# Kernel optimization log

Measured on AMD Instinct MI355X. Metric: run time of the kernel, lower is better.

Reference implementation:

```python
import jax, jax.numpy as jnp
import numpy as np

B, N, D = 4, 2048, 512
H, DH = 8, 64
MLP = 2048
EPS = 1e-5


def setup_inputs() -> dict:
    key = jax.random.key(0)
    ks = jax.random.split(key, 8)
    s = lambda fan_in: 1.0 / np.sqrt(fan_in)
    return {
        "x": jax.random.normal(ks[0], (B, N, D), jnp.float32),
        "ln1_g": jnp.ones((D,), jnp.float32),
        "ln1_b": jnp.zeros((D,), jnp.float32),
        "Wqkv": jax.random.normal(ks[1], (D, 3 * H * DH), jnp.float32) * s(D),
        "temperature": jnp.asarray(np.log(DH ** -0.5), jnp.float32),
        "Wo": jax.random.normal(ks[2], (H * DH, D), jnp.float32) * s(H * DH),
        "bo": jnp.zeros((D,), jnp.float32),
        "ln2_g": jnp.ones((D,), jnp.float32),
        "ln2_b": jnp.zeros((D,), jnp.float32),
        "W1": jax.random.normal(ks[3], (D, MLP), jnp.float32) * s(D),
        "b1": jnp.zeros((MLP,), jnp.float32),
        "W2": jax.random.normal(ks[4], (MLP, D), jnp.float32) * s(MLP),
        "b2": jnp.zeros((D,), jnp.float32),
    }


def _layernorm(x, g, b):
    mu = jnp.mean(x, axis=-1, keepdims=True)
    var = jnp.var(x, axis=-1, keepdims=True)
    return (x - mu) * jax.lax.rsqrt(var + EPS) * g + b


def _lsa(x, Wqkv, temperature, Wo, bo):
    b, n, _ = x.shape
    qkv = x @ Wqkv  # [b, n, 3*H*DH]
    q, k, v = jnp.split(qkv, 3, axis=-1)
    rs = lambda t: t.reshape(b, n, H, DH).transpose(0, 2, 1, 3)  # b h n d
    q, k, v = rs(q), rs(k), rs(v)
    dots = jnp.einsum("bhnd,bhmd->bhnm", q, k) * jnp.exp(temperature)
    mask_value = -jnp.finfo(dots.dtype).max
    eye = jnp.eye(n, dtype=bool)
    dots = jnp.where(eye, mask_value, dots)  # mask diagonal (LSA)
    attn = jax.nn.softmax(dots, axis=-1)
    out = jnp.einsum("bhnm,bhmd->bhnd", attn, v)
    out = out.transpose(0, 2, 1, 3).reshape(b, n, H * DH)
    return out @ Wo + bo


def _ffn(x, W1, b1, W2, b2):
    h = jax.nn.gelu(x @ W1 + b1, approximate=False)
    return h @ W2 + b2


def reference(x, ln1_g, ln1_b, Wqkv, temperature, Wo, bo,
              ln2_g, ln2_b, W1, b1, W2, b2):
    y = _lsa(_layernorm(x, ln1_g, ln1_b), Wqkv, temperature, Wo, bo) + x
    z = _ffn(_layernorm(y, ln2_g, ln2_b), W1, b1, W2, b2) + y
    return (z, x)
```

## Files before the change

kernel.cpp:

```cpp
#include <hip/hip_runtime.h>
#include <math.h>

typedef __attribute__((ext_vector_type(4))) float f32x4;
typedef __attribute__((ext_vector_type(8))) short short8;

#define DEV __device__ __forceinline__

DEV short f2bf(float f){
  union { float f; unsigned u; } v; v.f = f;
  unsigned r = v.u + 0x7fffu + ((v.u >> 16) & 1u);
  return (short)(r >> 16);
}
DEV float bf2f(short s){
  union { unsigned u; float f; } v; v.u = ((unsigned)(unsigned short)s) << 16; return v.f;
}
DEV float exp2_hw(float x){ float r; asm("v_exp_f32 %0, %1" : "=v"(r) : "v"(x)); return r; }
DEV float rcp_hw(float x){ float r; asm("v_rcp_f32 %0, %1" : "=v"(r) : "v"(x)); return r; }
DEV unsigned cvtpk(float a, float b){
  unsigned r; asm("v_cvt_pk_bf16_f32 %0, %1, %2" : "=v"(r) : "v"(a), "v"(b)); return r;
}
DEV void gload_lds16(const short* src, short* lds){
  __builtin_amdgcn_global_load_lds(
      (const __attribute__((address_space(1))) void*)src,
      (__attribute__((address_space(3))) void*)lds, 16, 0, 0);
}

__global__ __launch_bounds__(256) void transpose_bf16_kernel(
    const float* __restrict__ W, short* __restrict__ Wt, int K, int N)
{
  __shared__ float tile[32][33];
  int nb = blockIdx.x * 32, kb = blockIdx.y * 32;
  int tx = threadIdx.x & 31, ty = threadIdx.x >> 5;
  #pragma unroll
  for (int i = ty; i < 32; i += 8)
    tile[i][tx] = W[(size_t)(kb + i) * N + nb + tx];
  __syncthreads();
  #pragma unroll
  for (int i = ty; i < 32; i += 8)
    Wt[(size_t)(nb + i) * K + kb + tx] = f2bf(tile[tx][i]);
}

template<int COPYX>
__global__ __launch_bounds__(256) void ln_kernel(
    const float* __restrict__ x, const float* __restrict__ g,
    const float* __restrict__ b, short* __restrict__ out,
    float* __restrict__ xcopy)
{
  int row  = blockIdx.x * 4 + (threadIdx.x >> 6);
  int lane = threadIdx.x & 63;
  const float* xr = x + (size_t)row * 512 + lane * 8;
  f32x4 v0 = *(const f32x4*)(xr);
  f32x4 v1 = *(const f32x4*)(xr + 4);
  float s  = (v0[0]+v0[1]+v0[2]+v0[3]) + (v1[0]+v1[1]+v1[2]+v1[3]);
  float sq = (v0[0]*v0[0]+v0[1]*v0[1]+v0[2]*v0[2]+v0[3]*v0[3])
           + (v1[0]*v1[0]+v1[1]*v1[1]+v1[2]*v1[2]+v1[3]*v1[3]);
  #pragma unroll
  for (int off = 1; off < 64; off <<= 1) {
    s  += __shfl_xor(s, off);
    sq += __shfl_xor(sq, off);
  }
  float mu  = s * (1.0f / 512.0f);
  float var = sq * (1.0f / 512.0f) - mu * mu;
  float rstd = rsqrtf(var + 1e-5f);
  f32x4 g0 = *(const f32x4*)(g + lane * 8);
  f32x4 g1 = *(const f32x4*)(g + lane * 8 + 4);
  f32x4 b0 = *(const f32x4*)(b + lane * 8);
  f32x4 b1 = *(const f32x4*)(b + lane * 8 + 4);
  float o[8];
  #pragma unroll
  for (int j = 0; j < 4; ++j) o[j]     = (v0[j] - mu) * rstd * g0[j] + b0[j];
  #pragma unroll
  for (int j = 0; j < 4; ++j) o[4 + j] = (v1[j] - mu) * rstd * g1[j] + b1[j];
  uint4 pk;
  pk.x = cvtpk(o[0], o[1]); pk.y = cvtpk(o[2], o[3]);
  pk.z = cvtpk(o[4], o[5]); pk.w = cvtpk(o[6], o[7]);
  *(uint4*)(out + (size_t)row * 512 + lane * 8) = pk;
  if (COPYX) {
    float* xc = xcopy + (size_t)row * 512 + lane * 8;
    *(f32x4*)(xc)     = v0;
    *(f32x4*)(xc + 4) = v1;
  }
}

template<int EPI, int BM, typename OutT>
__global__ __launch_bounds__(256) void gemm_bt_kernel(
    const short* __restrict__ A, const short* __restrict__ Bt,
    OutT* __restrict__ C, const float* __restrict__ bias,
    const float* __restrict__ resid, short* __restrict__ vt,
    int M, int N, int K)
{
  constexpr int MFR = BM / 32;
  constexpr int NFR = 4;
  constexpr int AI  = BM / 64;
  constexpr int BUF = BM * 32 + 128 * 32;
  __shared__ __align__(16) short smem[3 * BUF];

  int tid = threadIdx.x;
  int lane = tid & 63, wid = tid >> 6;
  int l16 = lane & 15, lq = lane >> 4;

  int gx = gridDim.x;
  int nwg = gx * gridDim.y;
  int orig = blockIdx.y * gx + blockIdx.x;
  int swz = (orig & 7) * (nwg >> 3) + (orig >> 3);
  int bn = swz % gx, bm = swz / gx;

  int wm = wid >> 1, wn = wid & 1;

  const short* gaP[AI];
  const short* gbP[2];
  #pragma unroll
  for (int i = 0; i < AI; ++i) {
    int gg = i * 4 + wid;
    gaP[i] = A + (size_t)(bm * BM + gg * 16 + l16) * K + lq * 8;
  }
  #pragma unroll
  for (int i = 0; i < 2; ++i) {
    int gg = i * 4 + wid;
    gbP[i] = Bt + (size_t)(bn * 128 + gg * 16 + l16) * K + lq * 8;
  }

  auto STAGE = [&](int bufi, int k0) {
    short* base = smem + bufi * BUF;
    #pragma unroll
    for (int i = 0; i < AI; ++i)
      gload_lds16(gaP[i] + k0, base + (i * 4 + wid) * 512);
    #pragma unroll
    for (int i = 0; i < 2; ++i)
      gload_lds16(gbP[i] + k0, base + BM * 32 + (i * 4 + wid) * 512);
  };

  f32x4 acc[MFR][NFR] = {};

  STAGE(0, 0);
  STAGE(1, 32);

  int nt = K >> 5;
  for (int t = 0; t < nt; ++t) {
    if (t + 1 < nt) {
      if constexpr (AI == 2) asm volatile("s_waitcnt vmcnt(4)" ::: "memory");
      else                   asm volatile("s_waitcnt vmcnt(3)" ::: "memory");
    } else {
      asm volatile("s_waitcnt vmcnt(0)" ::: "memory");
    }
    __builtin_amdgcn_s_barrier();
    __builtin_amdgcn_sched_barrier(0);
    if (t + 2 < nt) STAGE((t + 2) % 3, (t + 2) << 5);

    const short* base = smem + (t % 3) * BUF;
    short8 af[MFR], bfr[NFR];
    #pragma unroll
    for (int m = 0; m < MFR; ++m)
      af[m] = *(const short8*)(base + (wm * MFR + m) * 512 + lane * 8);
    #pragma unroll
    for (int n = 0; n < NFR; ++n)
      bfr[n] = *(const short8*)(base + BM * 32 + (wn * NFR + n) * 512 + lane * 8);
    __builtin_amdgcn_s_setprio(1);
    #pragma unroll
    for (int m = 0; m < MFR; ++m)
      #pragma unroll
      for (int n = 0; n < NFR; ++n)
        acc[m][n] = __builtin_amdgcn_mfma_f32_16x16x32_bf16(af[m], bfr[n], acc[m][n], 0, 0, 0);
    __builtin_amdgcn_s_setprio(0);
  }

  if (EPI == 3 && bn >= 8) {
    __syncthreads();
    short* T = smem;
    #pragma unroll
    for (int m = 0; m < MFR; ++m)
      #pragma unroll
      for (int n = 0; n < NFR; ++n) {
        int c = wn * 64 + n * 16 + l16;
        #pragma unroll
        for (int r = 0; r < 4; ++r) {
          int rowl = wm * 64 + m * 16 + lq * 4 + r;
          T[c * 128 + (rowl ^ ((c & 7) << 4))] = f2bf(acc[m][n][r]);
        }
      }
    __syncthreads();
    int b2 = bm >> 4;
    int nnb = (bm & 15) * 128;
    int tn = tid & 15;
    #pragma unroll
    for (int c8 = 0; c8 < 8; ++c8) {
      int c = c8 * 16 + (tid >> 4);
      short8 v = *(const short8*)(T + c * 128 + ((tn * 8) ^ ((c & 7) << 4)));
      if (tn & 1) {
        short8 w;
        #pragma unroll
        for (int j = 0; j < 8; ++j) w[j] = v[j ^ 4];
        v = w;
      }
      int c2 = bn * 128 + c - 1024;
      int bh = b2 * 8 + (c2 >> 6);
      int d  = c2 & 63;
      *(short8*)(vt + ((size_t)(bh * 64 + d)) * 2048 + nnb + tn * 8) = v;
    }
    return;
  }

  float bv[NFR];
  #pragma unroll
  for (int n = 0; n < NFR; ++n)
    bv[n] = (EPI == 0 || EPI == 3) ? 0.0f : bias[bn * 128 + (wn * NFR + n) * 16 + l16];

  #pragma unroll
  for (int m = 0; m < MFR; ++m) {
    #pragma unroll
    for (int r = 0; r < 4; ++r) {
      int row = bm * BM + (wm * MFR + m) * 16 + lq * 4 + r;
      #pragma unroll
      for (int n = 0; n < NFR; ++n) {
        int col = bn * 128 + (wn * NFR + n) * 16 + l16;
        float v = acc[m][n][r];
        if (EPI == 1 || EPI == 2) v += bv[n];
        if (EPI == 2) v = 0.5f * v * (1.0f + erff(v * 0.70710678f));
        if (EPI == 1) v += resid[(size_t)row * N + col];
        if constexpr (sizeof(OutT) == 2)
          ((short*)C)[(size_t)row * N + col] = f2bf(v);
        else
          ((float*)C)[(size_t)row * N + col] = v;
      }
    }
  }
}

__global__ __launch_bounds__(256, 2) void attn_kernel(
    const short* __restrict__ qkv, const short* __restrict__ vt,
    const float* __restrict__ temp_ptr, short* __restrict__ out)
{
  __shared__ __align__(16) short smem[24576];

  int tid = threadIdx.x;
  int lane = tid & 63, wid = tid >> 6;
  int l16 = lane & 15, lq = lane >> 4;
  int hi = lq >> 1, lq0 = lq & 1;

  int orig = blockIdx.y * 16 + blockIdx.x;
  int swz = (orig & 7) * 64 + (orig >> 3);
  int qb = swz & 15, bh = swz >> 4;
  int b = bh >> 3, h = bh & 7;

  const short* qbase = qkv + (size_t)b * 2048 * 1536 + h * 64;
  const short* kbase = qbase + 512;
  const short* vbase = vt + (size_t)bh * 64 * 2048;

  float scale = __expf(temp_ptr[0]) * 1.44269504f;
  int q0 = qb * 128 + wid * 32;

  short8 qfrag[2][2];
  #pragma unroll
  for (int qf = 0; qf < 2; ++qf) {
    int qrow = q0 + qf * 16 + l16;
    #pragma unroll
    for (int c = 0; c < 2; ++c) {
      short8 raw = *(const short8*)(qbase + (size_t)qrow * 1536 + c * 32 + lq * 8);
      short8 sc;
      #pragma unroll
      for (int j = 0; j < 8; ++j) sc[j] = f2bf(bf2f(raw[j]) * scale);
      qfrag[qf][c] = sc;
    }
  }

  f32x4 accO[2][4] = {};
  float l[2] = {0.f, 0.f};

  auto STAGE = [&](int bufi, int k0) {
    #pragma unroll
    for (int i = 0; i < 2; ++i) {
      int w16 = i * 256 + tid;
      int sub = w16 >> 7;
      int cc  = (w16 >> 6) & 1;
      int lq2 = (w16 >> 4) & 3;
      int l2  = w16 & 15;
      const short* srcK = kbase + (size_t)(k0 + sub * 16 + l2) * 1536 + cc * 32 + lq2 * 8;
      gload_lds16(srcK, smem + bufi * 4096 + (i * 4 + wid) * 512);
      const short* srcV = vbase + (size_t)(sub * 16 + l2) * 2048 + k0 + cc * 32 + lq2 * 8;
      gload_lds16(srcV, smem + 12288 + bufi * 4096 + (i * 4 + wid) * 512);
    }
  };

  STAGE(0, 0);
  STAGE(1, 64);

  for (int t = 0; t < 32; ++t) {
    if (t + 1 < 32) asm volatile("s_waitcnt vmcnt(4)" ::: "memory");
    else            asm volatile("s_waitcnt vmcnt(0)" ::: "memory");
    __builtin_amdgcn_s_barrier();
    __builtin_amdgcn_sched_barrier(0);
    if (t + 2 < 32) STAGE((t + 2) % 3, (t + 2) * 64);

    int k0 = t * 64;
    const short* kls = smem + (t % 3) * 4096;
    const short* vls = smem + 12288 + (t % 3) * 4096;

    f32x4 accS[2][4] = {};
    __builtin_amdgcn_s_setprio(1);
    #pragma unroll
    for (int s = 0; s < 4; ++s) {
      short8 kf0 = *(const short8*)(kls + (s * 2 + 0) * 512 + lane * 8);
      short8 kf1 = *(const short8*)(kls + (s * 2 + 1) * 512 + lane * 8);
      #pragma unroll
      for (int qf = 0; qf < 2; ++qf) {
        accS[qf][s] = __builtin_amdgcn_mfma_f32_16x16x32_bf16(kf0, qfrag[qf][0], accS[qf][s], 0, 0, 0);
        accS[qf][s] = __builtin_amdgcn_mfma_f32_16x16x32_bf16(kf1, qfrag[qf][1], accS[qf][s], 0, 0, 0);
      }
    }
    __builtin_amdgcn_s_setprio(0);

    if ((q0 & ~63) == k0) {
      #pragma unroll
      for (int qf = 0; qf < 2; ++qf) {
        int qg = q0 + qf * 16 + l16;
        #pragma unroll
        for (int s = 0; s < 4; ++s)
          #pragma unroll
          for (int r = 0; r < 4; ++r)
            if (k0 + s * 16 + lq * 4 + r == qg) accS[qf][s][r] = -30000.f;
      }
    }

    short8 pa[2][2];
    #pragma unroll
    for (int qf = 0; qf < 2; ++qf) {
      float sum = 0.f;
      unsigned W[4][2];
      #pragma unroll
      for (int s = 0; s < 4; ++s) {
        float p0 = exp2_hw(accS[qf][s][0]);
        float p1 = exp2_hw(accS[qf][s][1]);
        float p2 = exp2_hw(accS[qf][s][2]);
        float p3 = exp2_hw(accS[qf][s][3]);
        sum += (p0 + p1) + (p2 + p3);
        W[s][0] = cvtpk(p0, p1);
        W[s][1] = cvtpk(p2, p3);
      }
      sum += __shfl_xor(sum, 16);
      sum += __shfl_xor(sum, 32);
      l[qf] += sum;

      unsigned K0[2], S0[2], K2[2], S2[2], R0[2], R2[2];
      #pragma unroll
      for (int w = 0; w < 2; ++w) {
        K0[w] = hi ? W[1][w] : W[0][w];
        S0[w] = hi ? W[0][w] : W[1][w];
        K2[w] = hi ? W[3][w] : W[2][w];
        S2[w] = hi ? W[2][w] : W[3][w];
      }
      #pragma unroll
      for (int w = 0; w < 2; ++w) {
        R0[w] = (unsigned)__shfl_xor((int)S0[w], 32);
        R2[w] = (unsigned)__shfl_xor((int)S2[w], 32);
      }
      bool sw = (hi != lq0);
      unsigned FA[2], FB[2], sA[2], sB[2], GA[2], GB[2];
      #pragma unroll
      for (int w = 0; w < 2; ++w) {
        sA[w] = sw ? K0[w] : R0[w];  FA[w] = sw ? R0[w] : K0[w];
        sB[w] = sw ? K2[w] : R2[w];  FB[w] = sw ? R2[w] : K2[w];
      }
      #pragma unroll
      for (int w = 0; w < 2; ++w) {
        GA[w] = (unsigned)__shfl_xor((int)sA[w], 16);
        GB[w] = (unsigned)__shfl_xor((int)sB[w], 16);
      }
      union { unsigned u[4]; short8 s8; } p0u, p1u;
      p0u.u[0] = FA[0]; p0u.u[1] = FA[1]; p0u.u[2] = GA[0]; p0u.u[3] = GA[1];
      p1u.u[0] = FB[0]; p1u.u[1] = FB[1]; p1u.u[2] = GB[0]; p1u.u[3] = GB[1];
      pa[qf][0] = p0u.s8;
      pa[qf][1] = p1u.s8;
    }

    short8 vfr[4][2];
    #pragma unroll
    for (int d = 0; d < 4; ++d) {
      vfr[d][0] = *(const short8*)(vls + (d * 2 + 0) * 512 + lane * 8);
      vfr[d][1] = *(const short8*)(vls + (d * 2 + 1) * 512 + lane * 8);
    }
    __builtin_amdgcn_s_setprio(1);
    #pragma unroll
    for (int qf = 0; qf < 2; ++qf)
      #pragma unroll
      for (int d = 0; d < 4; ++d) {
        accO[qf][d] = __builtin_amdgcn_mfma_f32_16x16x32_bf16(vfr[d][0], pa[qf][0], accO[qf][d], 0, 0, 0);
        accO[qf][d] = __builtin_amdgcn_mfma_f32_16x16x32_bf16(vfr[d][1], pa[qf][1], accO[qf][d], 0, 0, 0);
      }
    __builtin_amdgcn_s_setprio(0);
  }

  #pragma unroll
  for (int qf = 0; qf < 2; ++qf) {
    float inv = rcp_hw(l[qf]);
    int qg = q0 + qf * 16 + l16;
    size_t rowoff = (size_t)(b * 2048 + qg) * 512 + h * 64;
    #pragma unroll
    for (int d = 0; d < 4; ++d) {
      unsigned w0 = cvtpk(accO[qf][d][0] * inv, accO[qf][d][1] * inv);
      unsigned w1 = cvtpk(accO[qf][d][2] * inv, accO[qf][d][3] * inv);
      uint2 pk; pk.x = w0; pk.y = w1;
      *(uint2*)(out + rowoff + d * 16 + lq * 4) = pk;
    }
  }
}

extern "C" void kernel_launch(void* const* d_in, const int* in_sizes, int n_in,
                              void* d_out, int out_size, void* d_ws, size_t ws_size,
                              hipStream_t stream)
{
  const float* x    = (const float*)d_in[0];
  const float* ln1g = (const float*)d_in[1];
  const float* ln1b = (const float*)d_in[2];
  const float* Wqkv = (const float*)d_in[3];
  const float* temp = (const float*)d_in[4];
  const float* Wo   = (const float*)d_in[5];
  const float* bo   = (const float*)d_in[6];
  const float* ln2g = (const float*)d_in[7];
  const float* ln2b = (const float*)d_in[8];
  const float* W1   = (const float*)d_in[9];
  const float* b1   = (const float*)d_in[10];
  const float* W2   = (const float*)d_in[11];
  const float* b2   = (const float*)d_in[12];
  float* out = (float*)d_out;

  char* ws = (char*)d_ws;
  short* wqkv_t = (short*)(ws);
  short* wo_t   = (short*)(ws + 1572864);
  short* w1_t   = (short*)(ws + 2097152);
  short* w2_t   = (short*)(ws + 4194304);
  short* h      = (short*)(ws + 6291456);
  short* qkv    = (short*)(ws + 14680064);
  short* attn   = (short*)(ws + 39845888);
  float* y      = (float*)(ws + 48234496);
  short* vt     = (short*)(ws + 48234496);
  short* t      = (short*)(ws + 14680064);

  const int M = 8192;

  transpose_bf16_kernel<<<dim3(1536 / 32, 512 / 32),  256, 0, stream>>>(Wqkv, wqkv_t, 512, 1536);
  transpose_bf16_kernel<<<dim3(512 / 32, 512 / 32),   256, 0, stream>>>(Wo,   wo_t,   512, 512);
  transpose_bf16_kernel<<<dim3(2048 / 32, 512 / 32),  256, 0, stream>>>(W1,   w1_t,   512, 2048);
  transpose_bf16_kernel<<<dim3(512 / 32, 2048 / 32),  256, 0, stream>>>(W2,   w2_t,   2048, 512);

  ln_kernel<1><<<M / 4, 256, 0, stream>>>(x, ln1g, ln1b, h, out + (size_t)M * 512);

  gemm_bt_kernel<3, 128, short><<<dim3(1536 / 128, M / 128), 256, 0, stream>>>(
      h, wqkv_t, qkv, nullptr, nullptr, vt, M, 1536, 512);

  attn_kernel<<<dim3(16, 32), 256, 0, stream>>>(qkv, vt, temp, attn);

  gemm_bt_kernel<1, 64, float><<<dim3(512 / 128, M / 64), 256, 0, stream>>>(
      attn, wo_t, y, bo, x, nullptr, M, 512, 512);

  ln_kernel<0><<<M / 4, 256, 0, stream>>>(y, ln2g, ln2b, h, nullptr);

  gemm_bt_kernel<2, 128, short><<<dim3(2048 / 128, M / 128), 256, 0, stream>>>(
      h, w1_t, t, b1, nullptr, nullptr, M, 2048, 512);

  gemm_bt_kernel<1, 64, float><<<dim3(512 / 128, M / 64), 256, 0, stream>>>(
      t, w2_t, out, b2, y, nullptr, M, 512, 2048);
}
```

Before: 223.9 us.

## Load K/V fragments directly from global into registers in attention kernel

Removes the LDS triple-buffered staging of K and V tiles with global_load_lds and barriers, and has each wave load its K and V MFMA fragments straight from global memory into registers. K for the next tile is prefetched into registers after the QK MFMAs, and V is loaded at the top of each iteration. This drops the LDS footprint and block-wide barriers but makes each of the four waves re-read the same K/V data from global/L2 with less coalesced, strided 16-byte accesses. The occupancy hint is also relaxed.

```diff
diff --git a/kernel.cpp b/kernel.cpp
--- a/kernel.cpp
+++ b/kernel.cpp
@@ -226,12 +226,10 @@
   }
 }
 
-__global__ __launch_bounds__(256, 2) void attn_kernel(
+__global__ __launch_bounds__(256) void attn_kernel(
     const short* __restrict__ qkv, const short* __restrict__ vt,
     const float* __restrict__ temp_ptr, short* __restrict__ out)
 {
-  __shared__ __align__(16) short smem[24576];
-
   int tid = threadIdx.x;
   int lane = tid & 63, wid = tid >> 6;
   int l16 = lane & 15, lq = lane >> 4;
@@ -263,51 +261,46 @@
     }
   }
 
+  const short* kp = kbase + (size_t)l16 * 1536 + lq * 8;
+  const short* vp = vbase + (size_t)l16 * 2048 + lq * 8;
+
   f32x4 accO[2][4] = {};
   float l[2] = {0.f, 0.f};
 
-  auto STAGE = [&](int bufi, int k0) {
-    #pragma unroll
-    for (int i = 0; i < 2; ++i) {
-      int w16 = i * 256 + tid;
-      int sub = w16 >> 7;
-      int cc  = (w16 >> 6) & 1;
-      int lq2 = (w16 >> 4) & 3;
-      int l2  = w16 & 15;
-      const short* srcK = kbase + (size_t)(k0 + sub * 16 + l2) * 1536 + cc * 32 + lq2 * 8;
-      gload_lds16(srcK, smem + bufi * 4096 + (i * 4 + wid) * 512);
-      const short* srcV = vbase + (size_t)(sub * 16 + l2) * 2048 + k0 + cc * 32 + lq2 * 8;
-      gload_lds16(srcV, smem + 12288 + bufi * 4096 + (i * 4 + wid) * 512);
-    }
-  };
-
-  STAGE(0, 0);
-  STAGE(1, 64);
-
+  short8 kf[4][2];
+  #pragma unroll
+  for (int s = 0; s < 4; ++s)
+    #pragma unroll
+    for (int c = 0; c < 2; ++c)
+      kf[s][c] = *(const short8*)(kp + (size_t)(s * 16) * 1536 + c * 32);
+
+  #pragma unroll 2
   for (int t = 0; t < 32; ++t) {
-    if (t + 1 < 32) asm volatile("s_waitcnt vmcnt(4)" ::: "memory");
-    else            asm volatile("s_waitcnt vmcnt(0)" ::: "memory");
-    __builtin_amdgcn_s_barrier();
-    __builtin_amdgcn_sched_barrier(0);
-    if (t + 2 < 32) STAGE((t + 2) % 3, (t + 2) * 64);
-
     int k0 = t * 64;
-    const short* kls = smem + (t % 3) * 4096;
-    const short* vls = smem + 12288 + (t % 3) * 4096;
+
+    short8 vfr[4][2];
+    #pragma unroll
+    for (int d = 0; d < 4; ++d)
+      #pragma unroll
+      for (int c = 0; c < 2; ++c)
+        vfr[d][c] = *(const short8*)(vp + (size_t)(d * 16) * 2048 + k0 + c * 32);
 
     f32x4 accS[2][4] = {};
-    __builtin_amdgcn_s_setprio(1);
-    #pragma unroll
-    for (int s = 0; s < 4; ++s) {
-      short8 kf0 = *(const short8*)(kls + (s * 2 + 0) * 512 + lane * 8);
-      short8 kf1 = *(const short8*)(kls + (s * 2 + 1) * 512 + lane * 8);
+    #pragma unroll
+    for (int s = 0; s < 4; ++s)
       #pragma unroll
       for (int qf = 0; qf < 2; ++qf) {
-        accS[qf][s] = __builtin_amdgcn_mfma_f32_16x16x32_bf16(kf0, qfrag[qf][0], accS[qf][s], 0, 0, 0);
-        accS[qf][s] = __builtin_amdgcn_mfma_f32_16x16x32_bf16(kf1, qfrag[qf][1], accS[qf][s], 0, 0, 0);
-      }
-    }
-    __builtin_amdgcn_s_setprio(0);
+        accS[qf][s] = __builtin_amdgcn_mfma_f32_16x16x32_bf16(kf[s][0], qfrag[qf][0], accS[qf][s], 0, 0, 0);
+        accS[qf][s] = __builtin_amdgcn_mfma_f32_16x16x32_bf16(kf[s][1], qfrag[qf][1], accS[qf][s], 0, 0, 0);
+      }
+
+    if (t + 1 < 32) {
+      #pragma unroll
+      for (int s = 0; s < 4; ++s)
+        #pragma unroll
+        for (int c = 0; c < 2; ++c)
+          kf[s][c] = *(const short8*)(kp + (size_t)((t + 1) * 64 + s * 16) * 1536 + c * 32);
+    }
 
     if ((q0 & ~63) == k0) {
       #pragma unroll
@@ -372,13 +365,6 @@
       pa[qf][1] = p1u.s8;
     }
 
-    short8 vfr[4][2];
-    #pragma unroll
-    for (int d = 0; d < 4; ++d) {
-      vfr[d][0] = *(const short8*)(vls + (d * 2 + 0) * 512 + lane * 8);
-      vfr[d][1] = *(const short8*)(vls + (d * 2 + 1) * 512 + lane * 8);
-    }
-    __builtin_amdgcn_s_setprio(1);
     #pragma unroll
     for (int qf = 0; qf < 2; ++qf)
       #pragma unroll
@@ -386,7 +372,6 @@
         accO[qf][d] = __builtin_amdgcn_mfma_f32_16x16x32_bf16(vfr[d][0], pa[qf][0], accO[qf][d], 0, 0, 0);
         accO[qf][d] = __builtin_amdgcn_mfma_f32_16x16x32_bf16(vfr[d][1], pa[qf][1], accO[qf][d], 0, 0, 0);
       }
-    __builtin_amdgcn_s_setprio(0);
   }
 
   #pragma unroll
```

After: 286.6 us. +28.0%, slower.
